# Kernel tuning notes

Measured on AMD Instinct MI355X. Metric: run time of the kernel, lower is better.

Reference implementation:

```python
import jax, jax.numpy as jnp
import numpy as np

B, C, H, W = 8, 512, 128, 128   # batch, ham_channels, feature-map H, W
S, R = 1, 64                    # md_s, md_r
EVAL_STEPS = 7
EPS = 1e-6


def conv1x1(x, w, b):
    # x: [B,C,H,W], w: [O,C] (1x1 conv kernel), b: [O]
    return jnp.einsum('bchw,oc->bohw', x, w) + b[None, :, None, None]


def _update_coef(x, bases, coef):
    # x: [B,D,N], bases: [B,D,R], coef: [B,N,R]
    num = jnp.einsum('bdn,bdr->bnr', x, bases)
    btb = jnp.einsum('bdr,bds->brs', bases, bases)          # [B,R,R]
    den = jnp.einsum('bnr,brs->bns', coef, btb)
    return coef * num / (den + EPS)


def nmf2d(x, bases):
    # Multiplicative-update NMF, eval path (inv_t = 1).
    coef = jax.nn.softmax(jnp.einsum('bdn,bdr->bnr', x, bases), axis=-1)

    def step(carry, _):
        bases, coef = carry
        coef = _update_coef(x, bases, coef)
        num = jnp.einsum('bdn,bnr->bdr', x, coef)
        ctc = jnp.einsum('bnr,bns->brs', coef, coef)        # [B,R,R]
        den = jnp.einsum('bdr,brs->bds', bases, ctc)
        bases = bases * num / (den + EPS)
        return (bases, coef), None

    (bases, coef), _ = jax.lax.scan(step, (bases, coef), None, length=EVAL_STEPS)
    coef = _update_coef(x, bases, coef)                      # compute_coef
    return jnp.einsum('bdr,bnr->bdn', bases, coef)           # bases @ coef^T


def setup_inputs() -> dict:
    key = jax.random.key(0)
    ks = jax.random.split(key, 5)
    x = jax.random.normal(ks[0], (B, C, H, W), jnp.float32)
    w_in = jax.random.normal(ks[1], (C, C), jnp.float32) * 0.02
    b_in = jnp.zeros((C,), jnp.float32)
    w_out = jax.random.normal(ks[2], (C, C), jnp.float32) * 0.02
    b_out = jnp.zeros((C,), jnp.float32)
    bases = jax.random.uniform(ks[3], (S, C // S, R), jnp.float32)
    # f.normalize(..., dim=1): L2-normalize over channel dim
    bases = bases / jnp.maximum(jnp.linalg.norm(bases, axis=1, keepdims=True), 1e-12)
    return {'x': x, 'w_in': w_in, 'b_in': b_in, 'w_out': w_out, 'b_out': b_out, 'bases': bases}


def reference(x, w_in, b_in, w_out, b_out, bases):
    # ham_in (1x1 conv) + relu
    h = jax.nn.relu(conv1x1(x, w_in, b_in))
    # NMF2D: view to [B*s, C/s, H*W], repeat bases over batch
    xf = h.reshape(B * S, C // S, H * W)
    bb = jnp.tile(bases, (B, 1, 1))                          # [B*s, C/s, R]
    y = nmf2d(xf, bb).reshape(B, C, H, W)
    # ham_out (1x1 conv, no norm) + residual relu
    y = conv1x1(y, w_out, b_out)
    return jax.nn.relu(x + y)
```

## Files before the change

### kernel.cpp

```cpp
#include <hip/hip_runtime.h>
#include <hip/hip_bf16.h>

#define B_ 8
#define C_ 512
#define N_ 16384
#define R_ 64
#define EPS 1e-6f

typedef float  f32x4  __attribute__((ext_vector_type(4)));
typedef short  bf16x4 __attribute__((ext_vector_type(4)));
typedef short  bf16x8 __attribute__((ext_vector_type(8)));

#define DI __device__ __forceinline__

DI short f2bf(float f) {
    union { float f; unsigned u; } a; a.f = f;
    unsigned r = a.u + 0x7fffu + ((a.u >> 16) & 1u);
    return (short)(r >> 16);
}
DI float bf2f(short s) {
    union { unsigned u; float f; } a;
    a.u = ((unsigned)(unsigned short)s) << 16;
    return a.f;
}
DI unsigned pk2(float lo, float hi) {
    union { __hip_bfloat162 h; unsigned u; } c;
    c.h = __float22bfloat162_rn(make_float2(lo, hi));
    return c.u;
}

union BV { bf16x8 v; bf16x4 h[2]; };
DI bf16x8 ldfrag(const short* p) {
    BV u;
    u.h[0] = *(const bf16x4*)p;
    u.h[1] = *(const bf16x4*)(p + 4);
    return u.v;
}
DI f32x4 mfma16(bf16x8 a, bf16x8 b, f32x4 c) {
    return __builtin_amdgcn_mfma_f32_16x16x32_bf16(a, b, c, 0, 0, 0);
}

__global__ __launch_bounds__(256)
void k_prep(const float* __restrict__ bases, float* __restrict__ basesT,
            short* __restrict__ basesTb, const float* __restrict__ w_in,
            short* __restrict__ wbf) {
    int idx = blockIdx.x * 256 + threadIdx.x;
    const int d = idx & 511;
    const int r = (idx >> 9) & 63;
    const float v = bases[d * 64 + r];
    basesT[idx]  = v;
    basesTb[idx] = f2bf(v);
    wbf[idx] = f2bf(w_in[idx]);
}

__global__ __launch_bounds__(256)
void k_conv1(const short* __restrict__ Wbf, const float* __restrict__ bias,
             const float* __restrict__ X, short* __restrict__ Ht) {
    const int nb = blockIdx.x * 128, mb = blockIdx.y * 128, bb = blockIdx.z;
    const float* Xb = X + (size_t)bb * C_ * N_;
    short* HtB = Ht + (size_t)bb * N_ * C_;
    __shared__ short As[128 * 36];
    __shared__ short Bs[128 * 36];
    const int t = threadIdx.x;
    const int lane = t & 63, wave = t >> 6;
    const int wm = wave >> 1, wn = wave & 1;
    const int fr = lane & 15, fg = lane >> 4;
    f32x4 zero4 = {0.f, 0.f, 0.f, 0.f};
    f32x4 acc[4][4];
    for (int i = 0; i < 4; i++) for (int j = 0; j < 4; j++) acc[i][j] = zero4;

    const int an_row = t >> 2, an_kc = (t & 3) * 8;
    const int bkp = t >> 4;

    for (int kb = 0; kb < C_; kb += 32) {
        {
#pragma unroll
            for (int i = 0; i < 2; i++) {
                const int row = an_row + 64 * i;
                const short* src = Wbf + (size_t)(mb + row) * C_ + kb + an_kc;
                short* dst = &As[row * 36 + an_kc];
                *(bf16x4*)dst = *(const bf16x4*)src;
                *(bf16x4*)(dst + 4) = *(const bf16x4*)(src + 4);
            }
        }
        {
#pragma unroll
            for (int i = 0; i < 2; i++) {
                const int n0 = 4 * ((t & 15) + 16 * i);
                const float* r0 = Xb + (size_t)(kb + 2 * bkp) * N_ + nb + n0;
                float4 va = *(const float4*)r0;
                float4 vb = *(const float4*)(r0 + N_);
                const float* pa = (const float*)&va;
                const float* pb = (const float*)&vb;
#pragma unroll
                for (int j = 0; j < 4; j++)
                    *(unsigned*)&Bs[(n0 + j) * 36 + 2 * bkp] = pk2(pa[j], pb[j]);
            }
        }
        __syncthreads();
        bf16x8 af[4], bv[4];
#pragma unroll
        for (int mi = 0; mi < 4; mi++) af[mi] = ldfrag(&As[(wm * 64 + mi * 16 + fr) * 36 + fg * 8]);
#pragma unroll
        for (int ni = 0; ni < 4; ni++) bv[ni] = ldfrag(&Bs[(wn * 64 + ni * 16 + fr) * 36 + fg * 8]);
#pragma unroll
        for (int mi = 0; mi < 4; mi++)
#pragma unroll
            for (int ni = 0; ni < 4; ni++)
                acc[mi][ni] = mfma16(af[mi], bv[ni], acc[mi][ni]);
        __syncthreads();
    }
#pragma unroll
    for (int mi = 0; mi < 4; mi++) {
        const int c0 = mb + wm * 64 + mi * 16 + fg * 4;
        const float4 b4 = *(const float4*)&bias[c0];
        const float* bp = (const float*)&b4;
#pragma unroll
        for (int ni = 0; ni < 4; ni++) {
            const int n = nb + wn * 64 + ni * 16 + fr;
            bf16x4 pk;
#pragma unroll
            for (int j = 0; j < 4; j++) {
                float v = acc[mi][ni][j] + bp[j];
                pk[j] = f2bf(v > 0.f ? v : 0.f);
            }
            *(bf16x4*)&HtB[(size_t)n * C_ + c0] = pk;
        }
    }
}

template<int UPDATE>
__global__ __launch_bounds__(256)
void k_coef(const short* __restrict__ basesTb, const short* __restrict__ Ht,
            const short* __restrict__ btb, short* __restrict__ coef) {
    const int nb = blockIdx.x * 256, bb = blockIdx.y;
    const short* HtB = Ht + (size_t)bb * N_ * C_;
    const short* bT = basesTb + (size_t)bb * R_ * C_;
    short* coefB = coef + (size_t)bb * R_ * N_;
    __shared__ short As[64 * 36];
    __shared__ short Bs[256 * 44];
    __shared__ short Ds[64 * 68];
    const int t = threadIdx.x;
    const int lane = t & 63, wave = t >> 6;
    const int fr = lane & 15, fg = lane >> 4;
    f32x4 zero4 = {0.f, 0.f, 0.f, 0.f};
    f32x4 accN[4][4];
    for (int i = 0; i < 4; i++) for (int j = 0; j < 4; j++) accN[i][j] = zero4;

    for (int kb = 0; kb < C_; kb += 32) {
        {
            const int row = t >> 2, kc = (t & 3) * 8;
            const short* src = bT + row * C_ + kb + kc;
            short* dst = &As[row * 36 + kc];
            *(bf16x4*)dst = *(const bf16x4*)src;
            *(bf16x4*)(dst + 4) = *(const bf16x4*)(src + 4);
        }
        {
            const short* src = HtB + (size_t)(nb + t) * C_ + kb;
            short* dst = &Bs[t * 44];
#pragma unroll
            for (int s = 0; s < 4; s++) {
                BV u; u.v = *(const bf16x8*)(src + 8 * s);
                *(bf16x4*)(dst + 8 * s) = u.h[0];
                *(bf16x4*)(dst + 8 * s + 4) = u.h[1];
            }
        }
        __syncthreads();
        bf16x8 hf[4], bfr[4];
#pragma unroll
        for (int nt = 0; nt < 4; nt++) hf[nt] = ldfrag(&Bs[(wave * 64 + nt * 16 + fr) * 44 + fg * 8]);
#pragma unroll
        for (int rt = 0; rt < 4; rt++) bfr[rt] = ldfrag(&As[(rt * 16 + fr) * 36 + fg * 8]);
#pragma unroll
        for (int nt = 0; nt < 4; nt++)
#pragma unroll
            for (int rt = 0; rt < 4; rt++)
                accN[nt][rt] = mfma16(hf[nt], bfr[rt], accN[nt][rt]);
        __syncthreads();
    }

    if (UPDATE) {
        f32x4 accD[4][4];
        for (int i = 0; i < 4; i++) for (int j = 0; j < 4; j++) accD[i][j] = zero4;
        {
            const short* bt = btb + bb * R_ * R_;
#pragma unroll
            for (int i = 0; i < 2; i++) {
                const int row = t & 63, kc8 = ((t >> 6) + 4 * i) * 8;
                const short* src = bt + row * 64 + kc8;
                short* dst = &Ds[row * 68 + kc8];
                *(bf16x4*)dst = *(const bf16x4*)src;
                *(bf16x4*)(dst + 4) = *(const bf16x4*)(src + 4);
            }
        }
        for (int ks = 0; ks < 2; ks++) {
            const int sp = t >> 4;
            const int s0 = ks * 32 + 2 * sp;
#pragma unroll
            for (int p = 0; p < 8; p++) {
                const int n0 = 2 * ((t & 15) + 16 * p);
                const unsigned ra = *(const unsigned*)(coefB + (size_t)s0 * N_ + nb + n0);
                const unsigned rb = *(const unsigned*)(coefB + (size_t)(s0 + 1) * N_ + nb + n0);
                *(unsigned*)&Bs[n0 * 44 + 2 * sp] = (ra & 0xffffu) | (rb << 16);
                *(unsigned*)&Bs[(n0 + 1) * 44 + 2 * sp] = (ra >> 16) | (rb & 0xffff0000u);
            }
            __syncthreads();
            bf16x8 cf[4], df[4];
#pragma unroll
            for (int nt = 0; nt < 4; nt++) cf[nt] = ldfrag(&Bs[(wave * 64 + nt * 16 + fr) * 44 + fg * 8]);
#pragma unroll
            for (int rt = 0; rt < 4; rt++) df[rt] = ldfrag(&Ds[(rt * 16 + fr) * 68 + ks * 32 + fg * 8]);
#pragma unroll
            for (int nt = 0; nt < 4; nt++)
#pragma unroll
                for (int rt = 0; rt < 4; rt++)
                    accD[nt][rt] = mfma16(cf[nt], df[rt], accD[nt][rt]);
            __syncthreads();
        }
#pragma unroll
        for (int nt = 0; nt < 4; nt++)
#pragma unroll
            for (int rt = 0; rt < 4; rt++) {
                const int r = rt * 16 + fr;
                const int n0 = nb + wave * 64 + nt * 16 + fg * 4;
                short* p = coefB + (size_t)r * N_ + n0;
                bf16x4 old = *(const bf16x4*)p;
                bf16x4 nw;
#pragma unroll
                for (int j = 0; j < 4; j++)
                    nw[j] = f2bf(bf2f(old[j]) * accN[nt][rt][j] / (accD[nt][rt][j] + EPS));
                *(bf16x4*)p = nw;
            }
    } else {
#pragma unroll
        for (int nt = 0; nt < 4; nt++) {
            float mx[4], sm[4];
#pragma unroll
            for (int j = 0; j < 4; j++) {
                float m = accN[nt][0][j];
#pragma unroll
                for (int rt = 1; rt < 4; rt++) m = fmaxf(m, accN[nt][rt][j]);
                m = fmaxf(m, __shfl_xor(m, 1, 64));
                m = fmaxf(m, __shfl_xor(m, 2, 64));
                m = fmaxf(m, __shfl_xor(m, 4, 64));
                m = fmaxf(m, __shfl_xor(m, 8, 64));
                mx[j] = m; sm[j] = 0.f;
            }
#pragma unroll
            for (int rt = 0; rt < 4; rt++)
#pragma unroll
                for (int j = 0; j < 4; j++) {
                    float e = __expf(accN[nt][rt][j] - mx[j]);
                    accN[nt][rt][j] = e;
                    sm[j] += e;
                }
#pragma unroll
            for (int j = 0; j < 4; j++) {
                float s = sm[j];
                s += __shfl_xor(s, 1, 64);
                s += __shfl_xor(s, 2, 64);
                s += __shfl_xor(s, 4, 64);
                s += __shfl_xor(s, 8, 64);
                sm[j] = 1.f / s;
            }
#pragma unroll
            for (int rt = 0; rt < 4; rt++) {
                const int r = rt * 16 + fr;
                const int n0 = nb + wave * 64 + nt * 16 + fg * 4;
                bf16x4 pk;
#pragma unroll
                for (int j = 0; j < 4; j++) pk[j] = f2bf(accN[nt][rt][j] * sm[j]);
                *(bf16x4*)&coefB[(size_t)r * N_ + n0] = pk;
            }
        }
    }
}

template<int MODE>
__global__ __launch_bounds__(256)
void k_tn(const short* __restrict__ coef, const short* __restrict__ Ht,
          const short* __restrict__ basesTb, const float* __restrict__ Wout,
          float* __restrict__ parts, short* __restrict__ btb, short* __restrict__ wf) {
    const int ddt = blockIdx.x, ch = blockIdx.y, bb = blockIdx.z;
    const int kLen = (MODE == 0) ? 2048 : 512;
    const int k0g = ch * kLen;
    const short* Ap; int lda;
    if (MODE == 0) { Ap = coef + (size_t)bb * R_ * N_; lda = N_; }
    else           { Ap = basesTb + (size_t)bb * R_ * C_; lda = C_; }
    const short* HtB = Ht + (size_t)bb * N_ * C_;
    __shared__ short As[64 * 68];
    __shared__ short Bs[64 * 68];
    const int t = threadIdx.x;
    const int lane = t & 63, wave = t >> 6;
    const int fr = lane & 15, fg = lane >> 4;
    f32x4 zero4 = {0.f, 0.f, 0.f, 0.f};
    f32x4 acc[4];
    for (int i = 0; i < 4; i++) acc[i] = zero4;

    for (int kb = 0; kb < kLen; kb += 64) {
#pragma unroll
        for (int i = 0; i < 2; i++) {
            const int kg = (t & 7) * 8, row = (t >> 3) + 32 * i;
            const short* src = Ap + (size_t)row * lda + k0g + kb + kg;
            short* dst = &As[row * 68 + kg];
            *(bf16x4*)dst = *(const bf16x4*)src;
            *(bf16x4*)(dst + 4) = *(const bf16x4*)(src + 4);
        }
        if (MODE == 0 && ddt < 8) {
            const int dd0 = 2 * (t & 31);
#pragma unroll
            for (int i = 0; i < 4; i++) {
                const int n0 = 2 * ((t >> 5) + 8 * i);
                const unsigned ra = *(const unsigned*)(HtB + (size_t)(k0g + kb + n0) * C_ + ddt * 64 + dd0);
                const unsigned rb = *(const unsigned*)(HtB + (size_t)(k0g + kb + n0 + 1) * C_ + ddt * 64 + dd0);
                *(unsigned*)&Bs[dd0 * 68 + n0] = (ra & 0xffffu) | (rb << 16);
                *(unsigned*)&Bs[(dd0 + 1) * 68 + n0] = (ra >> 16) | (rb & 0xffff0000u);
            }
        } else {
#pragma unroll
            for (int i = 0; i < 2; i++) {
                const int kg = (t & 7) * 8, row = (t >> 3) + 32 * i;
                const int dd = ddt * 64 + row;
                short* dst = &Bs[row * 68 + kg];
                if (MODE == 2) {
                    const float* src = Wout + (size_t)dd * C_ + kb + kg;
                    float4 v0 = *(const float4*)src;
                    float4 v1 = *(const float4*)(src + 4);
                    *(unsigned*)dst = pk2(v0.x, v0.y);
                    *(unsigned*)(dst + 2) = pk2(v0.z, v0.w);
                    *(unsigned*)(dst + 4) = pk2(v1.x, v1.y);
                    *(unsigned*)(dst + 6) = pk2(v1.z, v1.w);
                } else {
                    const short* src;
                    if (MODE == 0)
                        src = coef + (size_t)bb * R_ * N_ + (size_t)(ddt * 64 + row - C_) * N_ + k0g + kb + kg;
                    else
                        src = basesTb + (size_t)bb * R_ * C_ + (size_t)dd * C_ + kb + kg;
                    *(bf16x4*)dst = *(const bf16x4*)src;
                    *(bf16x4*)(dst + 4) = *(const bf16x4*)(src + 4);
                }
            }
        }
        __syncthreads();
#pragma unroll
        for (int kk = 0; kk < 2; kk++) {
            bf16x8 a = ldfrag(&As[(wave * 16 + fr) * 68 + kk * 32 + fg * 8]);
#pragma unroll
            for (int ni = 0; ni < 4; ni++) {
                bf16x8 b = ldfrag(&Bs[(ni * 16 + fr) * 68 + kk * 32 + fg * 8]);
                acc[ni] = mfma16(a, b, acc[ni]);
            }
        }
        __syncthreads();
    }
    if (MODE == 2) {
#pragma unroll
        for (int ni = 0; ni < 4; ni++) {
            const int dd = ddt * 64 + ni * 16 + fr;
            const int r0 = wave * 16 + fg * 4;
            bf16x4 pk;
#pragma unroll
            for (int j = 0; j < 4; j++) pk[j] = f2bf(acc[ni][j]);
            *(bf16x4*)&wf[(size_t)bb * C_ * R_ + (size_t)dd * 64 + r0] = pk;
        }
    } else {
#pragma unroll
        for (int ni = 0; ni < 4; ni++)
#pragma unroll
            for (int j = 0; j < 4; j++) {
                const int r = wave * 16 + fg * 4 + j;
                const int dd = ddt * 64 + ni * 16 + fr;
                if (MODE == 0)
                    parts[(((size_t)bb * 8 + ch) * 64 + r) * 576 + dd] = acc[ni][j];
                else
                    btb[bb * R_ * R_ + r * 64 + dd] = f2bf(acc[ni][j]);
            }
    }
}

__global__ __launch_bounds__(256)
void k_bases_update(const float* __restrict__ parts, float* __restrict__ basesT,
                    short* __restrict__ basesTb) {
    const int dt = blockIdx.x, bb = blockIdx.y;
    __shared__ float ctcL[64 * 64];
    const int t = threadIdx.x;
    for (int idx = t; idx < 4096; idx += 256) {
        const int r = idx >> 6, s = idx & 63;
        float sum = 0.f;
#pragma unroll
        for (int ch = 0; ch < 8; ch++)
            sum += parts[(((size_t)bb * 8 + ch) * 64 + r) * 576 + 512 + s];
        ctcL[idx] = sum;
    }
    __syncthreads();
    float nv[16];
#pragma unroll
    for (int i = 0; i < 16; i++) {
        const int idx = t + i * 256;
        const int r = idx >> 6, d = dt * 64 + (idx & 63);
        float num = 0.f;
#pragma unroll
        for (int ch = 0; ch < 8; ch++)
            num += parts[(((size_t)bb * 8 + ch) * 64 + r) * 576 + d];
        float den = 0.f;
        const float* bcol = basesT + (size_t)bb * R_ * C_ + d;
        for (int s = 0; s < 64; s++)
            den += ctcL[r * 64 + s] * bcol[(size_t)s * C_];
        const float oldv = basesT[(size_t)bb * R_ * C_ + (size_t)r * C_ + d];
        nv[i] = oldv * num / (den + EPS);
    }
    __syncthreads();
#pragma unroll
    for (int i = 0; i < 16; i++) {
        const int idx = t + i * 256;
        const int r = idx >> 6, d = dt * 64 + (idx & 63);
        basesT[(size_t)bb * R_ * C_ + (size_t)r * C_ + d] = nv[i];
        basesTb[(size_t)bb * R_ * C_ + (size_t)r * C_ + d] = f2bf(nv[i]);
    }
}

__global__ __launch_bounds__(256)
void k_final(const short* __restrict__ wf, const short* __restrict__ coef,
             const float* __restrict__ X, const float* __restrict__ bias,
             float* __restrict__ out) {
    const int nb = blockIdx.x * 128, mb = blockIdx.y * 128, bb = blockIdx.z;
    __shared__ short As[128 * 68];
    __shared__ short Bs[128 * 68];
    const int t = threadIdx.x;
    const int lane = t & 63, wave = t >> 6;
    const int wm = wave >> 1, wn = wave & 1;
    const int fr = lane & 15, fg = lane >> 4;
    const short* wfb = wf + (size_t)bb * C_ * R_;
    const short* coefB = coef + (size_t)bb * R_ * N_;
    f32x4 zero4 = {0.f, 0.f, 0.f, 0.f};
    f32x4 acc[4][4];
    for (int i = 0; i < 4; i++) for (int j = 0; j < 4; j++) acc[i][j] = zero4;

#pragma unroll
    for (int i = 0; i < 4; i++) {
        const int kg = (t & 7) * 8, row = (t >> 3) + 32 * i;
        const short* src = wfb + (size_t)(mb + row) * 64 + kg;
        short* dst = &As[row * 68 + kg];
        *(bf16x4*)dst = *(const bf16x4*)src;
        *(bf16x4*)(dst + 4) = *(const bf16x4*)(src + 4);
    }
    {
        const int bn = 2 * (t & 15), bkp = t >> 4;
#pragma unroll
        for (int i = 0; i < 2; i++) {
            const int kp = bkp + 16 * i;
            const short* r0 = coefB + (size_t)(2 * kp) * N_ + nb + bn;
#pragma unroll
            for (int p = 0; p < 4; p++) {
                const unsigned ra = *(const unsigned*)(r0 + 32 * p);
                const unsigned rb = *(const unsigned*)(r0 + 32 * p + N_);
                *(unsigned*)&Bs[(bn + 32 * p) * 68 + 2 * kp] = (ra & 0xffffu) | (rb << 16);
                *(unsigned*)&Bs[(bn + 1 + 32 * p) * 68 + 2 * kp] = (ra >> 16) | (rb & 0xffff0000u);
            }
        }
    }
    __syncthreads();
#pragma unroll
    for (int kk = 0; kk < 2; kk++) {
        bf16x8 cf[4], af[4];
#pragma unroll
        for (int ni = 0; ni < 4; ni++) cf[ni] = ldfrag(&Bs[(wn * 64 + ni * 16 + fr) * 68 + kk * 32 + fg * 8]);
#pragma unroll
        for (int mi = 0; mi < 4; mi++) af[mi] = ldfrag(&As[(wm * 64 + mi * 16 + fr) * 68 + kk * 32 + fg * 8]);
#pragma unroll
        for (int ni = 0; ni < 4; ni++)
#pragma unroll
            for (int mi = 0; mi < 4; mi++)
                acc[ni][mi] = mfma16(cf[ni], af[mi], acc[ni][mi]);
    }
    const float* Xb = X + (size_t)bb * C_ * N_;
    float* Ob = out + (size_t)bb * C_ * N_;
#pragma unroll
    for (int mi = 0; mi < 4; mi++) {
        const int m = mb + wm * 64 + mi * 16 + fr;
        const float bvv = bias[m];
#pragma unroll
        for (int ni = 0; ni < 4; ni++) {
            const int n0 = nb + wn * 64 + ni * 16 + fg * 4;
            float4 xv = *(const float4*)&Xb[(size_t)m * N_ + n0];
            const float* xp = (const float*)&xv;
            float4 ov;
            float* op = (float*)&ov;
#pragma unroll
            for (int j = 0; j < 4; j++) {
                float v = xp[j] + acc[ni][mi][j] + bvv;
                op[j] = v > 0.f ? v : 0.f;
            }
            *(float4*)&Ob[(size_t)m * N_ + n0] = ov;
        }
    }
}

extern "C" void kernel_launch(void* const* d_in, const int* in_sizes, int n_in,
                              void* d_out, int out_size, void* d_ws, size_t ws_size,
                              hipStream_t stream) {
    const float* x     = (const float*)d_in[0];
    const float* w_in  = (const float*)d_in[1];
    const float* b_in  = (const float*)d_in[2];
    const float* w_out = (const float*)d_in[3];
    const float* b_out = (const float*)d_in[4];
    const float* bases = (const float*)d_in[5];
    float* out = (float*)d_out;

    short* ht      = (short*)d_ws;
    short* coef    = ht + (size_t)67108864;
    float* basesT  = (float*)(coef + 8388608);
    short* basesTb = (short*)(basesT + 262144);
    short* btb     = basesTb + 262144;
    short* wf      = btb + 32768;
    float* parts   = (float*)(wf + 262144);
    short* wbf     = (short*)(parts + 2359296);

    k_prep<<<1024, 256, 0, stream>>>(bases, basesT, basesTb, w_in, wbf);
    k_conv1<<<dim3(128, 4, 8), 256, 0, stream>>>(wbf, b_in, x, ht);
    k_coef<0><<<dim3(64, 8), 256, 0, stream>>>(basesTb, ht, btb, coef);
    for (int s = 0; s < 7; s++) {
        k_tn<1><<<dim3(1, 1, 8), 256, 0, stream>>>(coef, ht, basesTb, w_out, parts, btb, wf);
        k_coef<1><<<dim3(64, 8), 256, 0, stream>>>(basesTb, ht, btb, coef);
        k_tn<0><<<dim3(9, 8, 8), 256, 0, stream>>>(coef, ht, basesTb, w_out, parts, btb, wf);
        k_bases_update<<<dim3(8, 8), 256, 0, stream>>>(parts, basesT, basesTb);
    }
    k_tn<1><<<dim3(1, 1, 8), 256, 0, stream>>>(coef, ht, basesTb, w_out, parts, btb, wf);
    k_coef<1><<<dim3(64, 8), 256, 0, stream>>>(basesTb, ht, btb, coef);
    k_tn<2><<<dim3(8, 1, 8), 256, 0, stream>>>(coef, ht, basesTb, w_out, parts, btb, wf);
    k_final<<<dim3(128, 4, 8), 256, 0, stream>>>(wf, coef, x, b_out, out);
}
```

Baseline: 1.600 ms.

## Double-buffer shared memory with register prefetch in conv1, coef and reduction GEMMs

Converts the main K loops of the input conv, coefficient and reduction GEMM kernels to a two-stage pipeline. Each loop now prefetches the next tile's global data into registers while the current LDS buffer is consumed, then stores it into the alternate buffer. The aim is to overlap global load latency with MFMA work and to need one barrier per iteration instead of two. MODE 1 also reads the B operand from As, which holds the same bases tile, so that load is skipped. The cost is twice the LDS footprint and more registers, which may lower occupancy.

```diff
diff --git a/kernel.cpp b/kernel.cpp
--- a/kernel.cpp
+++ b/kernel.cpp
@@ -59,8 +59,8 @@
     const int nb = blockIdx.x * 128, mb = blockIdx.y * 128, bb = blockIdx.z;
     const float* Xb = X + (size_t)bb * C_ * N_;
     short* HtB = Ht + (size_t)bb * N_ * C_;
-    __shared__ short As[128 * 36];
-    __shared__ short Bs[128 * 36];
+    __shared__ short As[2][128 * 36];
+    __shared__ short Bs[2][128 * 36];
     const int t = threadIdx.x;
     const int lane = t & 63, wave = t >> 6;
     const int wm = wave >> 1, wn = wave & 1;
@@ -72,37 +72,57 @@
     const int an_row = t >> 2, an_kc = (t & 3) * 8;
     const int bkp = t >> 4;
 
-    for (int kb = 0; kb < C_; kb += 32) {
-        {
-#pragma unroll
-            for (int i = 0; i < 2; i++) {
-                const int row = an_row + 64 * i;
-                const short* src = Wbf + (size_t)(mb + row) * C_ + kb + an_kc;
-                short* dst = &As[row * 36 + an_kc];
-                *(bf16x4*)dst = *(const bf16x4*)src;
-                *(bf16x4*)(dst + 4) = *(const bf16x4*)(src + 4);
-            }
-        }
-        {
-#pragma unroll
-            for (int i = 0; i < 2; i++) {
-                const int n0 = 4 * ((t & 15) + 16 * i);
-                const float* r0 = Xb + (size_t)(kb + 2 * bkp) * N_ + nb + n0;
-                float4 va = *(const float4*)r0;
-                float4 vb = *(const float4*)(r0 + N_);
-                const float* pa = (const float*)&va;
-                const float* pb = (const float*)&vb;
-#pragma unroll
-                for (int j = 0; j < 4; j++)
-                    *(unsigned*)&Bs[(n0 + j) * 36 + 2 * bkp] = pk2(pa[j], pb[j]);
-            }
-        }
-        __syncthreads();
+    auto LD = [&](int kb, bf16x8 (&a)[2], float4 (&f)[4]) {
+#pragma unroll
+        for (int i = 0; i < 2; i++)
+            a[i] = *(const bf16x8*)(Wbf + (size_t)(mb + an_row + 64 * i) * C_ + kb + an_kc);
+#pragma unroll
+        for (int i = 0; i < 2; i++) {
+            const int n0 = 4 * ((t & 15) + 16 * i);
+            const float* r0 = Xb + (size_t)(kb + 2 * bkp) * N_ + nb + n0;
+            f[2 * i]     = *(const float4*)r0;
+            f[2 * i + 1] = *(const float4*)(r0 + N_);
+        }
+    };
+    auto ST = [&](short* Asb, short* Bsb, const bf16x8 (&a)[2], const float4 (&f)[4]) {
+#pragma unroll
+        for (int i = 0; i < 2; i++) {
+            BV u; u.v = a[i];
+            short* dst = &Asb[(an_row + 64 * i) * 36 + an_kc];
+            *(bf16x4*)dst = u.h[0]; *(bf16x4*)(dst + 4) = u.h[1];
+        }
+#pragma unroll
+        for (int i = 0; i < 2; i++) {
+            const int n0 = 4 * ((t & 15) + 16 * i);
+            const float* pa = (const float*)&f[2 * i];
+            const float* pb = (const float*)&f[2 * i + 1];
+#pragma unroll
+            for (int j = 0; j < 4; j++)
+                *(unsigned*)&Bsb[(n0 + j) * 36 + 2 * bkp] = pk2(pa[j], pb[j]);
+        }
+    };
+
+    bf16x8 a0[2], a1[2]; float4 f0[4], f1[4];
+    LD(0, a0, f0);
+    ST(As[0], Bs[0], a0, f0);
+    LD(32, a1, f1);
+    __syncthreads();
+
+#pragma unroll
+    for (int i = 0; i < 16; i++) {
+        const int cur = i & 1;
+        if (cur == 0) {
+            if (i < 15) ST(As[1], Bs[1], a1, f1);
+            if (i < 14) LD((i + 2) * 32, a0, f0);
+        } else {
+            if (i < 15) ST(As[0], Bs[0], a0, f0);
+            if (i < 14) LD((i + 2) * 32, a1, f1);
+        }
         bf16x8 af[4], bv[4];
 #pragma unroll
-        for (int mi = 0; mi < 4; mi++) af[mi] = ldfrag(&As[(wm * 64 + mi * 16 + fr) * 36 + fg * 8]);
-#pragma unroll
-        for (int ni = 0; ni < 4; ni++) bv[ni] = ldfrag(&Bs[(wn * 64 + ni * 16 + fr) * 36 + fg * 8]);
+        for (int mi = 0; mi < 4; mi++) af[mi] = ldfrag(&As[cur][(wm * 64 + mi * 16 + fr) * 36 + fg * 8]);
+#pragma unroll
+        for (int ni = 0; ni < 4; ni++) bv[ni] = ldfrag(&Bs[cur][(wn * 64 + ni * 16 + fr) * 36 + fg * 8]);
 #pragma unroll
         for (int mi = 0; mi < 4; mi++)
 #pragma unroll
@@ -137,8 +157,8 @@
     const short* HtB = Ht + (size_t)bb * N_ * C_;
     const short* bT = basesTb + (size_t)bb * R_ * C_;
     short* coefB = coef + (size_t)bb * R_ * N_;
-    __shared__ short As[64 * 36];
-    __shared__ short Bs[256 * 44];
+    __shared__ short As[2][64 * 36];
+    __shared__ short Bs[2][256 * 44];
     __shared__ short Ds[64 * 68];
     const int t = threadIdx.x;
     const int lane = t & 63, wave = t >> 6;
@@ -147,30 +167,48 @@
     f32x4 accN[4][4];
     for (int i = 0; i < 4; i++) for (int j = 0; j < 4; j++) accN[i][j] = zero4;
 
-    for (int kb = 0; kb < C_; kb += 32) {
-        {
-            const int row = t >> 2, kc = (t & 3) * 8;
-            const short* src = bT + row * C_ + kb + kc;
-            short* dst = &As[row * 36 + kc];
-            *(bf16x4*)dst = *(const bf16x4*)src;
-            *(bf16x4*)(dst + 4) = *(const bf16x4*)(src + 4);
-        }
-        {
-            const short* src = HtB + (size_t)(nb + t) * C_ + kb;
-            short* dst = &Bs[t * 44];
-#pragma unroll
-            for (int s = 0; s < 4; s++) {
-                BV u; u.v = *(const bf16x8*)(src + 8 * s);
-                *(bf16x4*)(dst + 8 * s) = u.h[0];
-                *(bf16x4*)(dst + 8 * s + 4) = u.h[1];
-            }
-        }
-        __syncthreads();
+    const int arow = t >> 2, akc = (t & 3) * 8;
+
+    auto LD1 = [&](int kb, bf16x8& a, bf16x8 (&b)[4]) {
+        a = *(const bf16x8*)(bT + arow * C_ + kb + akc);
+        const short* src = HtB + (size_t)(nb + t) * C_ + kb;
+#pragma unroll
+        for (int s = 0; s < 4; s++) b[s] = *(const bf16x8*)(src + 8 * s);
+    };
+    auto ST1 = [&](short* Asb, short* Bsb, bf16x8 a, const bf16x8 (&b)[4]) {
+        BV u; u.v = a;
+        short* ad = &Asb[arow * 36 + akc];
+        *(bf16x4*)ad = u.h[0]; *(bf16x4*)(ad + 4) = u.h[1];
+        short* dst = &Bsb[t * 44];
+#pragma unroll
+        for (int s = 0; s < 4; s++) {
+            BV w; w.v = b[s];
+            *(bf16x4*)(dst + 8 * s) = w.h[0];
+            *(bf16x4*)(dst + 8 * s + 4) = w.h[1];
+        }
+    };
+
+    bf16x8 a0, a1, b0[4], b1[4];
+    LD1(0, a0, b0);
+    ST1(As[0], Bs[0], a0, b0);
+    LD1(32, a1, b1);
+    __syncthreads();
+
+#pragma unroll
+    for (int i = 0; i < 16; i++) {
+        const int cur = i & 1;
+        if (cur == 0) {
+            if (i < 15) ST1(As[1], Bs[1], a1, b1);
+            if (i < 14) LD1((i + 2) * 32, a0, b0);
+        } else {
+            if (i < 15) ST1(As[0], Bs[0], a0, b0);
+            if (i < 14) LD1((i + 2) * 32, a1, b1);
+        }
         bf16x8 hf[4], bfr[4];
 #pragma unroll
-        for (int nt = 0; nt < 4; nt++) hf[nt] = ldfrag(&Bs[(wave * 64 + nt * 16 + fr) * 44 + fg * 8]);
-#pragma unroll
-        for (int rt = 0; rt < 4; rt++) bfr[rt] = ldfrag(&As[(rt * 16 + fr) * 36 + fg * 8]);
+        for (int nt = 0; nt < 4; nt++) hf[nt] = ldfrag(&Bs[cur][(wave * 64 + nt * 16 + fr) * 44 + fg * 8]);
+#pragma unroll
+        for (int rt = 0; rt < 4; rt++) bfr[rt] = ldfrag(&As[cur][(rt * 16 + fr) * 36 + fg * 8]);
 #pragma unroll
         for (int nt = 0; nt < 4; nt++)
 #pragma unroll
@@ -201,13 +239,13 @@
                 const int n0 = 2 * ((t & 15) + 16 * p);
                 const unsigned ra = *(const unsigned*)(coefB + (size_t)s0 * N_ + nb + n0);
                 const unsigned rb = *(const unsigned*)(coefB + (size_t)(s0 + 1) * N_ + nb + n0);
-                *(unsigned*)&Bs[n0 * 44 + 2 * sp] = (ra & 0xffffu) | (rb << 16);
-                *(unsigned*)&Bs[(n0 + 1) * 44 + 2 * sp] = (ra >> 16) | (rb & 0xffff0000u);
+                *(unsigned*)&Bs[0][n0 * 44 + 2 * sp] = (ra & 0xffffu) | (rb << 16);
+                *(unsigned*)&Bs[0][(n0 + 1) * 44 + 2 * sp] = (ra >> 16) | (rb & 0xffff0000u);
             }
             __syncthreads();
             bf16x8 cf[4], df[4];
 #pragma unroll
-            for (int nt = 0; nt < 4; nt++) cf[nt] = ldfrag(&Bs[(wave * 64 + nt * 16 + fr) * 44 + fg * 8]);
+            for (int nt = 0; nt < 4; nt++) cf[nt] = ldfrag(&Bs[0][(wave * 64 + nt * 16 + fr) * 44 + fg * 8]);
 #pragma unroll
             for (int rt = 0; rt < 4; rt++) df[rt] = ldfrag(&Ds[(rt * 16 + fr) * 68 + ks * 32 + fg * 8]);
 #pragma unroll
@@ -282,14 +320,15 @@
           const short* __restrict__ basesTb, const float* __restrict__ Wout,
           float* __restrict__ parts, short* __restrict__ btb, short* __restrict__ wf) {
     const int ddt = blockIdx.x, ch = blockIdx.y, bb = blockIdx.z;
-    const int kLen = (MODE == 0) ? 2048 : 512;
-    const int k0g = ch * kLen;
+    const int kSteps = (MODE == 0) ? 32 : 8;
+    const int k0g = ch * ((MODE == 0) ? 2048 : 512);
     const short* Ap; int lda;
     if (MODE == 0) { Ap = coef + (size_t)bb * R_ * N_; lda = N_; }
     else           { Ap = basesTb + (size_t)bb * R_ * C_; lda = C_; }
     const short* HtB = Ht + (size_t)bb * N_ * C_;
-    __shared__ short As[64 * 68];
-    __shared__ short Bs[64 * 68];
+    const short* coefB = coef + (size_t)bb * R_ * N_;
+    __shared__ short As[2][64 * 68];
+    __shared__ short Bs[2][64 * 68];
     const int t = threadIdx.x;
     const int lane = t & 63, wave = t >> 6;
     const int fr = lane & 15, fg = lane >> 4;
@@ -297,57 +336,103 @@
     f32x4 acc[4];
     for (int i = 0; i < 4; i++) acc[i] = zero4;
 
-    for (int kb = 0; kb < kLen; kb += 64) {
+    const int kg = (t & 7) * 8, rr = t >> 3;
+
+    struct TReg { bf16x8 a[2]; unsigned bu[8]; float4 bf[4]; };
+
+    auto LDT = [&](int kb, TReg& R) {
+#pragma unroll
+        for (int i = 0; i < 2; i++)
+            R.a[i] = *(const bf16x8*)(Ap + (size_t)(rr + 32 * i) * lda + k0g + kb + kg);
+        if (MODE == 0) {
+            if (ddt < 8) {
+                const int dd0 = 2 * (t & 31);
+#pragma unroll
+                for (int i = 0; i < 4; i++) {
+                    const int n0 = 2 * ((t >> 5) + 8 * i);
+                    R.bu[2 * i]     = *(const unsigned*)(HtB + (size_t)(k0g + kb + n0) * C_ + ddt * 64 + dd0);
+                    R.bu[2 * i + 1] = *(const unsigned*)(HtB + (size_t)(k0g + kb + n0 + 1) * C_ + ddt * 64 + dd0);
+                }
+            } else {
+#pragma unroll
+                for (int i = 0; i < 2; i++) {
+                    const unsigned* src = (const unsigned*)(coefB + (size_t)(rr + 32 * i) * N_ + k0g + kb + kg);
+#pragma unroll
+                    for (int q = 0; q < 4; q++) R.bu[4 * i + q] = src[q];
+                }
+            }
+        } else if (MODE == 2) {
+#pragma unroll
+            for (int i = 0; i < 2; i++) {
+                const float* src = Wout + (size_t)(ddt * 64 + rr + 32 * i) * C_ + kb + kg;
+                R.bf[2 * i]     = *(const float4*)src;
+                R.bf[2 * i + 1] = *(const float4*)(src + 4);
+            }
+        }
+    };
+    auto STT = [&](short* Asb, short* Bsb, const TReg& R) {
 #pragma unroll
         for (int i = 0; i < 2; i++) {
-            const int kg = (t & 7) * 8, row = (t >> 3) + 32 * i;
-            const short* src = Ap + (size_t)row * lda + k0g + kb + kg;
-            short* dst = &As[row * 68 + kg];
-            *(bf16x4*)dst = *(const bf16x4*)src;
-            *(bf16x4*)(dst + 4) = *(const bf16x4*)(src + 4);
-        }
-        if (MODE == 0 && ddt < 8) {
-            const int dd0 = 2 * (t & 31);
-#pragma unroll
-            for (int i = 0; i < 4; i++) {
-                const int n0 = 2 * ((t >> 5) + 8 * i);
-                const unsigned ra = *(const unsigned*)(HtB + (size_t)(k0g + kb + n0) * C_ + ddt * 64 + dd0);
-                const unsigned rb = *(const unsigned*)(HtB + (size_t)(k0g + kb + n0 + 1) * C_ + ddt * 64 + dd0);
-                *(unsigned*)&Bs[dd0 * 68 + n0] = (ra & 0xffffu) | (rb << 16);
-                *(unsigned*)&Bs[(dd0 + 1) * 68 + n0] = (ra >> 16) | (rb & 0xffff0000u);
-            }
+            BV u; u.v = R.a[i];
+            short* dst = &Asb[(rr + 32 * i) * 68 + kg];
+            *(bf16x4*)dst = u.h[0]; *(bf16x4*)(dst + 4) = u.h[1];
+        }
+        if (MODE == 0) {
+            if (ddt < 8) {
+                const int dd0 = 2 * (t & 31);
+#pragma unroll
+                for (int i = 0; i < 4; i++) {
+                    const int n0 = 2 * ((t >> 5) + 8 * i);
+                    const unsigned ra = R.bu[2 * i], rb = R.bu[2 * i + 1];
+                    *(unsigned*)&Bsb[dd0 * 68 + n0] = (ra & 0xffffu) | (rb << 16);
+                    *(unsigned*)&Bsb[(dd0 + 1) * 68 + n0] = (ra >> 16) | (rb & 0xffff0000u);
+                }
+            } else {
+#pragma unroll
+                for (int i = 0; i < 2; i++) {
+                    unsigned* dst = (unsigned*)&Bsb[(rr + 32 * i) * 68 + kg];
+#pragma unroll
+                    for (int q = 0; q < 4; q++) dst[q] = R.bu[4 * i + q];
+                }
+            }
+        } else if (MODE == 2) {
+#pragma unroll
+            for (int i = 0; i < 2; i++) {
+                short* dst = &Bsb[(rr + 32 * i) * 68 + kg];
+                const float* p0 = (const float*)&R.bf[2 * i];
+                const float* p1 = (const float*)&R.bf[2 * i + 1];
+                *(unsigned*)dst       = pk2(p0[0], p0[1]);
+                *(unsigned*)(dst + 2) = pk2(p0[2], p0[3]);
+                *(unsigned*)(dst + 4) = pk2(p1[0], p1[1]);
+                *(unsigned*)(dst + 6) = pk2(p1[2], p1[3]);
+            }
+        }
+    };
+
+    TReg R0, R1;
+    LDT(0, R0);
+    STT(As[0], Bs[0], R0);
+    LDT(64, R1);
+    __syncthreads();
+
+#pragma unroll
+    for (int i = 0; i < kSteps; i++) {
+        const int cur = i & 1;
+        if (cur == 0) {
+            if (i < kSteps - 1) STT(As[1], Bs[1], R1);
+            if (i < kSteps - 2) LDT((i + 2) * 64, R0);
         } else {
-#pragma unroll
-            for (int i = 0; i < 2; i++) {
-                const int kg = (t & 7) * 8, row = (t >> 3) + 32 * i;
-                const int dd = ddt * 64 + row;
-                short* dst = &Bs[row * 68 + kg];
-                if (MODE == 2) {
-                    const float* src = Wout + (size_t)dd * C_ + kb + kg;
-                    float4 v0 = *(const float4*)src;
-                    float4 v1 = *(const float4*)(src + 4);
-                    *(unsigned*)dst = pk2(v0.x, v0.y);
-                    *(unsigned*)(dst + 2) = pk2(v0.z, v0.w);
-                    *(unsigned*)(dst + 4) = pk2(v1.x, v1.y);
-                    *(unsigned*)(dst + 6) = pk2(v1.z, v1.w);
-                } else {
-                    const short* src;
-                    if (MODE == 0)
-                        src = coef + (size_t)bb * R_ * N_ + (size_t)(ddt * 64 + row - C_) * N_ + k0g + kb + kg;
-                    else
-                        src = basesTb + (size_t)bb * R_ * C_ + (size_t)dd * C_ + kb + kg;
-                    *(bf16x4*)dst = *(const bf16x4*)src;
-                    *(bf16x4*)(dst + 4) = *(const bf16x4*)(src + 4);
-                }
-            }
-        }
-        __syncthreads();
+            if (i < kSteps - 1) STT(As[0], Bs[0], R0);
+            if (i < kSteps - 2) LDT((i + 2) * 64, R1);
+        }
 #pragma unroll
         for (int kk = 0; kk < 2; kk++) {
-            bf16x8 a = ldfrag(&As[(wave * 16 + fr) * 68 + kk * 32 + fg * 8]);
+            bf16x8 a = ldfrag(&As[cur][(wave * 16 + fr) * 68 + kk * 32 + fg * 8]);
 #pragma unroll
             for (int ni = 0; ni < 4; ni++) {
-                bf16x8 b = ldfrag(&Bs[(ni * 16 + fr) * 68 + kk * 32 + fg * 8]);
+                const short* bp = (MODE == 1) ? &As[cur][(ni * 16 + fr) * 68 + kk * 32 + fg * 8]
+                                              : &Bs[cur][(ni * 16 + fr) * 68 + kk * 32 + fg * 8];
+                bf16x8 b = ldfrag(bp);
                 acc[ni] = mfma16(a, b, acc[ni]);
             }
         }
```

After: 1.570 ms. Within noise of the previous version (-1.9%).
